# Performance work log

Hardware: AMD Instinct MI355X
Metric: run time of the kernel (lower is better)

## Reference

```python
import jax, jax.numpy as jnp
import numpy as np

H = 32          # query heads
KV = 8          # kv heads
DH = 64         # head dim
WINDOW = 1024   # sliding window
BASE = 10000.0  # rope base


def _rope(x, pos):
    """Interleaved RoPE as in RotaryEmbedding.apply. x: (B,H,T,Dh), pos: (T,)."""
    inv = 1.0 / (BASE ** (jnp.arange(0, DH, 2, dtype=jnp.float32) / DH))  # (Dh/2,)
    freqs = pos.astype(jnp.float32)[:, None] * inv[None, :]               # (T, Dh/2)
    cos = jnp.cos(freqs)[None, None].astype(x.dtype)
    sin = jnp.sin(freqs)[None, None].astype(x.dtype)
    x1, x2 = x[..., ::2], x[..., 1::2]
    o1 = x1 * cos - x2 * sin
    o2 = x1 * sin + x2 * cos
    return jnp.stack([o1, o2], axis=-1).reshape(x.shape)


def setup_inputs() -> dict:
    key = jax.random.key(0)
    ks = jax.random.split(key, 5)
    B, T, D, Tc = 2, 4096, 2048, 4096
    x = jax.random.normal(ks[0], (B, T, D), jnp.float32)
    k_cache = jax.random.normal(ks[1], (B, KV, Tc, DH), jnp.float32)
    v_cache = jax.random.normal(ks[2], (B, KV, Tc, DH), jnp.float32)
    Wq = jax.random.normal(ks[3], (D, D), jnp.float32) * 0.02
    Wo = jax.random.normal(ks[4], (D, D), jnp.float32) * 0.02
    return {"x": x, "k_cache": k_cache, "v_cache": v_cache, "Wq": Wq, "Wo": Wo}


def reference(x, k_cache, v_cache, Wq, Wo):
    """AttnLayer.forward, role='follower', local=True, return_attn=False, eval mode."""
    B, T, D = x.shape
    rep = H // KV
    # q projection: nn.Linear(d, H*Dh, bias=False) -> x @ W.T
    q = (x @ Wq.T).reshape(B, T, H, DH).transpose(0, 2, 1, 3)  # (B,H,T,Dh)
    Tc = k_cache.shape[2]
    pos_q = jnp.arange(Tc - T, Tc)
    q = _rope(q, pos_q)
    # GQA: KV -> H head replication (repeat_interleave along head dim)
    k = jnp.repeat(k_cache, rep, axis=1)  # (B,H,Tc,Dh)
    v = jnp.repeat(v_cache, rep, axis=1)
    # sliding-window slice: keep last `window` keys
    w = min(WINDOW, Tc)
    k = k[:, :, Tc - w:, :]  # (B,H,Tk,Dh)
    v = v[:, :, Tc - w:, :]
    Tk = w
    scale = 1.0 / np.sqrt(DH).astype(np.float32)
    scores = jnp.einsum('bhtd,bhsd->bhts', q, k) * scale  # (B,H,T,Tk)
    # torch SDPA is_causal with L != S uses a TOP-LEFT aligned tril mask: j <= i
    causal = jnp.arange(Tk)[None, :] <= jnp.arange(T)[:, None]  # (T,Tk)
    scores = jnp.where(causal[None, None], scores, -jnp.inf)
    attn = jax.nn.softmax(scores, axis=-1)
    out = jnp.einsum('bhts,bhsd->bhtd', attn, v)
    out = out.transpose(0, 2, 1, 3).reshape(B, T, H * DH)
    return out @ Wo.T
```

## Files before the change

kernel.cpp:

```cpp
#include <hip/hip_runtime.h>
#include <math.h>

typedef __attribute__((ext_vector_type(8))) short short8;
typedef __attribute__((ext_vector_type(4))) float floatx4;
typedef __attribute__((ext_vector_type(4))) unsigned int uintx4;
typedef __attribute__((ext_vector_type(2))) unsigned int uintx2;

#define MFMA16(a, b, c) __builtin_amdgcn_mfma_f32_16x16x32_bf16((a), (b), (c), 0, 0, 0)

#define QSCALE 0.18033688011112042f

__device__ __forceinline__ unsigned short f2bf(float x) {
    unsigned int u = __float_as_uint(x);
    u += 0x7fffu + ((u >> 16) & 1u);
    return (unsigned short)(u >> 16);
}

__device__ __forceinline__ short8 lds8(const unsigned short* p) {
    return *reinterpret_cast<const short8*>(p);
}

__device__ __forceinline__ void g2l16(const unsigned short* g, unsigned short* l) {
    __builtin_amdgcn_global_load_lds(
        (const __attribute__((address_space(1))) unsigned int*)g,
        (__attribute__((address_space(3))) unsigned int*)l,
        16, 0, 0);
}

__device__ __forceinline__ unsigned int cvtpk(float a, float b) {
    unsigned int r;
    asm("v_cvt_pk_bf16_f32 %0, %1, %2" : "=v"(r) : "v"(a), "v"(b));
    return r;
}

__device__ __forceinline__ void pl32swap(unsigned int& a, unsigned int& b) {
    asm("v_permlane32_swap_b32 %0, %1" : "+v"(a), "+v"(b));
}

__device__ __forceinline__ void pl16swap(unsigned int& a, unsigned int& b) {
    asm("v_permlane16_swap_b32 %0, %1" : "+v"(a), "+v"(b));
}

__global__ void cvt_bf16(const float* __restrict__ src, unsigned short* __restrict__ dst, int n4) {
    int i = blockIdx.x * blockDim.x + threadIdx.x;
    if (i >= n4) return;
    float4 v = reinterpret_cast<const float4*>(src)[i];
    ushort4 o;
    o.x = f2bf(v.x); o.y = f2bf(v.y); o.z = f2bf(v.z); o.w = f2bf(v.w);
    reinterpret_cast<ushort4*>(dst)[i] = o;
}

__global__ void prep_k(const float* __restrict__ kc, unsigned short* __restrict__ Kw) {
    int i = blockIdx.x * blockDim.x + threadIdx.x;
    int d4  = (i & 15) * 4;
    int s   = (i >> 4) & 1023;
    int bkv = i >> 14;
    size_t src = ((size_t)bkv * 4096 + 3072 + s) * 64 + d4;
    float4 kv = *reinterpret_cast<const float4*>(kc + src);
    ushort4 ko;
    ko.x = f2bf(kv.x); ko.y = f2bf(kv.y); ko.z = f2bf(kv.z); ko.w = f2bf(kv.w);
    *reinterpret_cast<ushort4*>(Kw + ((size_t)bkv * 1024 + s) * 64 + d4) = ko;
}

__global__ void prep_v(const float* __restrict__ vc, unsigned short* __restrict__ Vt) {
    __shared__ unsigned short tl[64][72];
    const int bkv = blockIdx.x >> 4;
    const int s0  = (blockIdx.x & 15) * 64;
    const int t   = threadIdx.x;
    const int sl  = t >> 2;
    const int dq  = (t & 3) * 16;
    const float* src = vc + ((size_t)bkv * 4096 + 3072 + s0 + sl) * 64 + dq;
    float4 v0 = reinterpret_cast<const float4*>(src)[0];
    float4 v1 = reinterpret_cast<const float4*>(src)[1];
    float4 v2 = reinterpret_cast<const float4*>(src)[2];
    float4 v3 = reinterpret_cast<const float4*>(src)[3];
    tl[dq +  0][sl] = f2bf(v0.x); tl[dq +  1][sl] = f2bf(v0.y);
    tl[dq +  2][sl] = f2bf(v0.z); tl[dq +  3][sl] = f2bf(v0.w);
    tl[dq +  4][sl] = f2bf(v1.x); tl[dq +  5][sl] = f2bf(v1.y);
    tl[dq +  6][sl] = f2bf(v1.z); tl[dq +  7][sl] = f2bf(v1.w);
    tl[dq +  8][sl] = f2bf(v2.x); tl[dq +  9][sl] = f2bf(v2.y);
    tl[dq + 10][sl] = f2bf(v2.z); tl[dq + 11][sl] = f2bf(v2.w);
    tl[dq + 12][sl] = f2bf(v3.x); tl[dq + 13][sl] = f2bf(v3.y);
    tl[dq + 14][sl] = f2bf(v3.z); tl[dq + 15][sl] = f2bf(v3.w);
    __syncthreads();
    const int dl = t >> 2;
    const int sc = (t & 3) * 16;
    unsigned short* dst = Vt + ((size_t)bkv * 64 + dl) * 1024 + s0 + sc;
    short8 x0 = *reinterpret_cast<const short8*>(&tl[dl][sc]);
    short8 x1 = *reinterpret_cast<const short8*>(&tl[dl][sc + 8]);
    *reinterpret_cast<short8*>(dst)     = x0;
    *reinterpret_cast<short8*>(dst + 8) = x1;
}

template <int EPI>
__global__ __launch_bounds__(256)
void gemm_bt(const unsigned short* __restrict__ A,
             const unsigned short* __restrict__ Bt,
             float* __restrict__ Cf,
             unsigned short* __restrict__ Cb) {
    constexpr int K = 2048;
    __shared__ unsigned short As[128 * 32];
    __shared__ unsigned short Bs[128 * 32];
    __shared__ float2 tab[EPI == 0 ? 128 * 33 : 1];

    const int tid  = threadIdx.x;
    const int lane = tid & 63;
    const int l15  = lane & 15;
    const int quad = lane >> 4;
    const int wid  = tid >> 6;
    const int wm   = (wid & 1) * 64;
    const int wn   = (wid >> 1) * 64;

    const int bn = blockIdx.x & 15;
    const int bm = blockIdx.x >> 4;

    if (EPI == 0) {
        const int t0 = (bm & 31) * 128;
        for (int e = tid; e < 4096; e += 256) {
            int tl = e >> 5, d2 = e & 31;
            float f = (float)(t0 + tl) * exp2f(-(float)d2 * 0.41524101186092f);
            float sn, cs; __sincosf(f, &sn, &cs);
            tab[tl * 33 + d2] = make_float2(cs, sn);
        }
    }

    const int row0 = tid >> 2;
    const int kc8  = (tid & 3) * 8;
    const unsigned short* Ag0 = A  + (size_t)(bm * 128 + row0) * K + kc8;
    const unsigned short* Ag1 = Ag0 + (size_t)64 * K;
    const unsigned short* Bg0 = Bt + (size_t)(bn * 128 + row0) * K + kc8;
    const unsigned short* Bg1 = Bg0 + (size_t)64 * K;
    unsigned short* AsW0 = As + wid * 512;
    unsigned short* AsW1 = As + 2048 + wid * 512;
    unsigned short* BsW0 = Bs + wid * 512;
    unsigned short* BsW1 = Bs + 2048 + wid * 512;

    floatx4 c00 = {0,0,0,0}, c01 = {0,0,0,0}, c02 = {0,0,0,0}, c03 = {0,0,0,0};
    floatx4 c10 = {0,0,0,0}, c11 = {0,0,0,0}, c12 = {0,0,0,0}, c13 = {0,0,0,0};
    floatx4 c20 = {0,0,0,0}, c21 = {0,0,0,0}, c22 = {0,0,0,0}, c23 = {0,0,0,0};
    floatx4 c30 = {0,0,0,0}, c31 = {0,0,0,0}, c32 = {0,0,0,0}, c33 = {0,0,0,0};

    for (int k0 = 0; k0 < K; k0 += 32) {
        __syncthreads();
        g2l16(Ag0 + k0, AsW0);
        g2l16(Ag1 + k0, AsW1);
        g2l16(Bg0 + k0, BsW0);
        g2l16(Bg1 + k0, BsW1);
        __syncthreads();

        short8 a0 = lds8(&As[(wm +  0 + l15) * 32 + quad * 8]);
        short8 a1 = lds8(&As[(wm + 16 + l15) * 32 + quad * 8]);
        short8 a2 = lds8(&As[(wm + 32 + l15) * 32 + quad * 8]);
        short8 a3 = lds8(&As[(wm + 48 + l15) * 32 + quad * 8]);
        short8 b0 = lds8(&Bs[(wn +  0 + l15) * 32 + quad * 8]);
        short8 b1 = lds8(&Bs[(wn + 16 + l15) * 32 + quad * 8]);
        short8 b2 = lds8(&Bs[(wn + 32 + l15) * 32 + quad * 8]);
        short8 b3 = lds8(&Bs[(wn + 48 + l15) * 32 + quad * 8]);

        c00 = MFMA16(a0, b0, c00); c01 = MFMA16(a0, b1, c01);
        c02 = MFMA16(a0, b2, c02); c03 = MFMA16(a0, b3, c03);
        c10 = MFMA16(a1, b0, c10); c11 = MFMA16(a1, b1, c11);
        c12 = MFMA16(a1, b2, c12); c13 = MFMA16(a1, b3, c13);
        c20 = MFMA16(a2, b0, c20); c21 = MFMA16(a2, b1, c21);
        c22 = MFMA16(a2, b2, c22); c23 = MFMA16(a2, b3, c23);
        c30 = MFMA16(a3, b0, c30); c31 = MFMA16(a3, b1, c31);
        c32 = MFMA16(a3, b2, c32); c33 = MFMA16(a3, b3, c33);
    }

#define EPI_TILE(i, j, C) do {                                                  \
    _Pragma("unroll")                                                           \
    for (int r = 0; r < 4; ++r) {                                               \
        int row = bm * 128 + wm + (i) * 16 + quad * 4 + r;                      \
        int col = bn * 128 + wn + (j) * 16 + l15;                               \
        float v = (C)[r];                                                       \
        if (EPI == 0) {                                                         \
            float p = __shfl_xor(v, 1);                                         \
            int t = row & 4095, b = row >> 12;                                  \
            int hh = col >> 6, d = col & 63;                                    \
            int tl = wm + (i) * 16 + quad * 4 + r;                              \
            float2 cspair = tab[tl * 33 + (d >> 1)];                            \
            float o = (d & 1) ? (p * cspair.y + v * cspair.x)                   \
                              : (v * cspair.x - p * cspair.y);                  \
            o *= QSCALE;                                                        \
            float po = __shfl_xor(o, 1);                                        \
            if (!(lane & 1)) {                                                  \
                unsigned int pk = (unsigned int)f2bf(o) |                       \
                                  ((unsigned int)f2bf(po) << 16);               \
                *reinterpret_cast<unsigned int*>(                               \
                    Cb + ((size_t)((b * 32 + hh) * 4096 + t)) * 64 + d) = pk;   \
            }                                                                   \
        } else {                                                                \
            Cf[(size_t)row * 2048 + col] = v;                                   \
        }                                                                       \
    }                                                                           \
} while (0)

    EPI_TILE(0, 0, c00); EPI_TILE(0, 1, c01); EPI_TILE(0, 2, c02); EPI_TILE(0, 3, c03);
    EPI_TILE(1, 0, c10); EPI_TILE(1, 1, c11); EPI_TILE(1, 2, c12); EPI_TILE(1, 3, c13);
    EPI_TILE(2, 0, c20); EPI_TILE(2, 1, c21); EPI_TILE(2, 2, c22); EPI_TILE(2, 3, c23);
    EPI_TILE(3, 0, c30); EPI_TILE(3, 1, c31); EPI_TILE(3, 2, c32); EPI_TILE(3, 3, c33);
#undef EPI_TILE
}

__global__ __launch_bounds__(512, 8)
void attn(const unsigned short* __restrict__ Q,
          const unsigned short* __restrict__ Kw,
          const unsigned short* __restrict__ Vt,
          unsigned short* __restrict__ O) {
    const int blk  = blockIdx.x;
    const int qblk = blk & 31;
    const int bh   = blk >> 5;
    const int h    = bh & 31;
    const int b    = bh >> 5;
    const int kvh  = h >> 2;

    const int tid  = threadIdx.x;
    const int lane = tid & 63;
    const int l15  = lane & 15;
    const int quad = lane >> 4;
    const int wid  = tid >> 6;
    const int qt0  = qblk * 128 + wid * 16;

    const unsigned short* Qp = Q  + ((size_t)bh * 4096 + qt0) * 64;
    const unsigned short* Kp = Kw + (size_t)(b * 8 + kvh) * 1024 * 64;
    const unsigned short* Vp = Vt + (size_t)(b * 8 + kvh) * 64 * 1024;

    __shared__ unsigned short Ks[2][4096];
    __shared__ unsigned short Vs[2][4096];

    short8 qa0 = lds8(&Qp[l15 * 64 + quad * 8]);
    short8 qa1 = lds8(&Qp[l15 * 64 + 32 + quad * 8]);

    const unsigned short* gK = Kp + (size_t)((wid >> 1) * 16 + l15) * 64
                                  + (wid & 1) * 32 + quad * 8;
    const unsigned short* gV = Vp + (size_t)((wid >> 1) * 16 + l15) * 1024
                                  + (wid & 1) * 32 + quad * 8;
    unsigned short* sK0 = &Ks[0][wid * 512];
    unsigned short* sK1 = &Ks[1][wid * 512];
    unsigned short* sV0 = &Vs[0][wid * 512];
    unsigned short* sV1 = &Vs[1][wid * 512];

    const int ntiles = (qblk < 7 ? 2 * qblk + 2 : 16);
    const int nkW    = (qt0 + 16 < 1024) ? qt0 + 16 : 1024;
    const int ntW    = (nkW + 63) >> 6;
    const bool diagW = (qt0 < 1024);

    g2l16(gK, sK0);
    g2l16(gV, sV0);

    floatx4 o0 = {0,0,0,0}, o1 = {0,0,0,0}, o2 = {0,0,0,0}, o3 = {0,0,0,0};
    float Lq = 0.f;
    float m = -INFINITY;

    for (int it = 0; it < ntiles; ++it) {
        __syncthreads();
        const int cur = it & 1;
        if (it + 1 < ntiles) {
            g2l16(gK + (it + 1) * 4096, cur ? sK0 : sK1);
            g2l16(gV + (it + 1) * 64,   cur ? sV0 : sV1);
        }
        if (it >= ntW) continue;
        const int s0 = it << 6;
        const unsigned short* Kc = Ks[cur];
        const unsigned short* Vc = Vs[cur];

        floatx4 sS[4];
#pragma unroll
        for (int c = 0; c < 4; ++c) {
            floatx4 z = {0, 0, 0, 0};
            z = MFMA16(lds8(Kc + c * 1024 + lane * 8), qa0, z);
            z = MFMA16(lds8(Kc + c * 1024 + 512 + lane * 8), qa1, z);
            sS[c] = z;
        }

        const bool last = (it == ntW - 1);
        bool skipHi = false;
        if (last && diagW) {
#pragma unroll
            for (int c = 0; c < 4; ++c)
#pragma unroll
                for (int r = 0; r < 4; ++r)
                    if (s0 + c * 16 + quad * 4 + r > qt0 + l15) sS[c][r] = -INFINITY;
            skipHi = (nkW - s0 <= 32);
        }

        float t0 = fmaxf(fmaxf(sS[0][0], sS[0][1]), fmaxf(sS[0][2], sS[0][3]));
        float t1 = fmaxf(fmaxf(sS[1][0], sS[1][1]), fmaxf(sS[1][2], sS[1][3]));
        float t2 = fmaxf(fmaxf(sS[2][0], sS[2][1]), fmaxf(sS[2][2], sS[2][3]));
        float t3 = fmaxf(fmaxf(sS[3][0], sS[3][1]), fmaxf(sS[3][2], sS[3][3]));
        float mx = fmaxf(fmaxf(t0, t1), fmaxf(t2, t3));
        mx = fmaxf(mx, __shfl_xor(mx, 16));
        mx = fmaxf(mx, __shfl_xor(mx, 32));

        if (!__all(mx <= m + 8.0f)) {
            const float mn = fmaxf(m, mx);
            const float alpha = exp2f(m - mn);
            m = mn;
            o0 *= alpha; o1 *= alpha; o2 *= alpha; o3 *= alpha;
            Lq *= alpha;
        }

        float p[4][4];
#pragma unroll
        for (int c = 0; c < 4; ++c)
#pragma unroll
            for (int r = 0; r < 4; ++r) p[c][r] = exp2f(sS[c][r] - m);
        Lq += ((p[0][0] + p[0][1] + p[0][2] + p[0][3]) + (p[1][0] + p[1][1] + p[1][2] + p[1][3]))
            + ((p[2][0] + p[2][1] + p[2][2] + p[2][3]) + (p[3][0] + p[3][1] + p[3][2] + p[3][3]));

        unsigned int a0 = cvtpk(p[0][0], p[0][1]);
        unsigned int a1 = cvtpk(p[0][2], p[0][3]);
        unsigned int a2 = cvtpk(p[1][0], p[1][1]);
        unsigned int a3 = cvtpk(p[1][2], p[1][3]);
        pl32swap(a0, a2); pl32swap(a1, a3);
        pl16swap(a0, a2); pl16swap(a1, a3);
        uintx4 tlo = {a0, a1, a2, a3};
        short8 pa_lo = __builtin_bit_cast(short8, tlo);

        o0 = MFMA16(lds8(Vc + 0 * 512 + lane * 8), pa_lo, o0);
        o1 = MFMA16(lds8(Vc + 2 * 512 + lane * 8), pa_lo, o1);
        o2 = MFMA16(lds8(Vc + 4 * 512 + lane * 8), pa_lo, o2);
        o3 = MFMA16(lds8(Vc + 6 * 512 + lane * 8), pa_lo, o3);
        if (!skipHi) {
            unsigned int b0 = cvtpk(p[2][0], p[2][1]);
            unsigned int b1 = cvtpk(p[2][2], p[2][3]);
            unsigned int b2 = cvtpk(p[3][0], p[3][1]);
            unsigned int b3 = cvtpk(p[3][2], p[3][3]);
            pl32swap(b0, b2); pl32swap(b1, b3);
            pl16swap(b0, b2); pl16swap(b1, b3);
            uintx4 thi = {b0, b1, b2, b3};
            short8 pa_hi = __builtin_bit_cast(short8, thi);
            o0 = MFMA16(lds8(Vc + 1 * 512 + lane * 8), pa_hi, o0);
            o1 = MFMA16(lds8(Vc + 3 * 512 + lane * 8), pa_hi, o1);
            o2 = MFMA16(lds8(Vc + 5 * 512 + lane * 8), pa_hi, o2);
            o3 = MFMA16(lds8(Vc + 7 * 512 + lane * 8), pa_hi, o3);
        }
    }

    Lq += __shfl_xor(Lq, 16);
    Lq += __shfl_xor(Lq, 32);
    const float inv = 1.f / Lq;

    unsigned short* Op = O + (size_t)b * 4096 * 2048 + (size_t)(qt0 + l15) * 2048
                           + h * 64 + quad * 4;
    uintx2 w0, w1, w2, w3;
    w0.x = cvtpk(o0[0] * inv, o0[1] * inv); w0.y = cvtpk(o0[2] * inv, o0[3] * inv);
    w1.x = cvtpk(o1[0] * inv, o1[1] * inv); w1.y = cvtpk(o1[2] * inv, o1[3] * inv);
    w2.x = cvtpk(o2[0] * inv, o2[1] * inv); w2.y = cvtpk(o2[2] * inv, o2[3] * inv);
    w3.x = cvtpk(o3[0] * inv, o3[1] * inv); w3.y = cvtpk(o3[2] * inv, o3[3] * inv);
    *reinterpret_cast<uintx2*>(Op)      = w0;
    *reinterpret_cast<uintx2*>(Op + 16) = w1;
    *reinterpret_cast<uintx2*>(Op + 32) = w2;
    *reinterpret_cast<uintx2*>(Op + 48) = w3;
}

extern "C" void kernel_launch(void* const* d_in, const int* in_sizes, int n_in,
                              void* d_out, int out_size, void* d_ws, size_t ws_size,
                              hipStream_t stream) {
    const float* x  = (const float*)d_in[0];
    const float* kc = (const float*)d_in[1];
    const float* vc = (const float*)d_in[2];
    const float* Wq = (const float*)d_in[3];
    const float* Wo = (const float*)d_in[4];
    float* out = (float*)d_out;

    char* ws = (char*)d_ws;
    unsigned short* Xb  = (unsigned short*)(ws);
    unsigned short* Qb  = (unsigned short*)(ws + 33554432);
    unsigned short* Wqb = (unsigned short*)(ws + 67108864);
    unsigned short* Wob = (unsigned short*)(ws + 75497472);
    unsigned short* Kwb = (unsigned short*)(ws + 83886080);
    unsigned short* Vtb = (unsigned short*)(ws + 85983232);

    cvt_bf16<<<16384, 256, 0, stream>>>(x,  Xb,  4194304);
    cvt_bf16<<<4096,  256, 0, stream>>>(Wq, Wqb, 1048576);
    cvt_bf16<<<4096,  256, 0, stream>>>(Wo, Wob, 1048576);
    prep_k<<<1024, 256, 0, stream>>>(kc, Kwb);
    prep_v<<<256, 256, 0, stream>>>(vc, Vtb);

    gemm_bt<0><<<1024, 256, 0, stream>>>(Xb, Wqb, nullptr, Qb);
    attn<<<2048, 512, 0, stream>>>(Qb, Kwb, Vtb, Xb);
    gemm_bt<1><<<1024, 256, 0, stream>>>(Xb, Wob, out, nullptr);
}
```

Measured before the change: 505.8 us.

## Replace GEMM with 256x256-tile double-buffered kernel using async LDS loads

```diff
diff --git a/kernel.cpp b/kernel.cpp
--- a/kernel.cpp
+++ b/kernel.cpp
@@ -93,113 +93,124 @@
 }
 
 template <int EPI>
-__global__ __launch_bounds__(256)
-void gemm_bt(const unsigned short* __restrict__ A,
+__global__ __launch_bounds__(512, 2)
+void gemm256(const unsigned short* __restrict__ A,
              const unsigned short* __restrict__ Bt,
              float* __restrict__ Cf,
              unsigned short* __restrict__ Cb) {
-    constexpr int K = 2048;
-    __shared__ unsigned short As[128 * 32];
-    __shared__ unsigned short Bs[128 * 32];
-    __shared__ float2 tab[EPI == 0 ? 128 * 33 : 1];
+    constexpr int K  = 2048;
+    constexpr int NT = 64;
+    __shared__ unsigned short sm[32768];
 
     const int tid  = threadIdx.x;
     const int lane = tid & 63;
     const int l15  = lane & 15;
     const int quad = lane >> 4;
     const int wid  = tid >> 6;
-    const int wm   = (wid & 1) * 64;
-    const int wn   = (wid >> 1) * 64;
-
-    const int bn = blockIdx.x & 15;
-    const int bm = blockIdx.x >> 4;
-
+    const int wr   = wid >> 2;
+    const int wc   = wid & 3;
+
+    const int bn = blockIdx.x & 7;
+    const int bm = blockIdx.x >> 3;
+
+    const unsigned short* gA0 = A  + (size_t)(bm * 256 + 2 * wid * 16 + l15) * K + quad * 8;
+    const unsigned short* gA1 = gA0 + (size_t)16 * K;
+    const unsigned short* gB0 = Bt + (size_t)(bn * 256 + 2 * wid * 16 + l15) * K + quad * 8;
+    const unsigned short* gB1 = gB0 + (size_t)16 * K;
+
+    auto STAGE = [&](int t) {
+        unsigned short* dst = sm + (t & 1) * 16384 + 2 * wid * 512;
+        const int off = t * 32;
+        g2l16(gA0 + off, dst);
+        g2l16(gA1 + off, dst + 512);
+        g2l16(gB0 + off, dst + 8192);
+        g2l16(gB1 + off, dst + 8704);
+    };
+
+    floatx4 acc[8][4];
+#pragma unroll
+    for (int i = 0; i < 8; ++i)
+#pragma unroll
+        for (int j = 0; j < 4; ++j) acc[i][j] = floatx4{0, 0, 0, 0};
+
+    STAGE(0);
+    STAGE(1);
+    asm volatile("s_waitcnt vmcnt(4)" ::: "memory");
+    __builtin_amdgcn_s_barrier();
+    asm volatile("" ::: "memory");
+
+    for (int t = 0; t < NT; ++t) {
+        const unsigned short* cb = sm + (t & 1) * 16384;
+
+        short8 bf[4], af[8];
+#pragma unroll
+        for (int j = 0; j < 4; ++j)
+            bf[j] = lds8(cb + 8192 + (wc * 4 + j) * 512 + lane * 8);
+#pragma unroll
+        for (int i = 0; i < 8; ++i)
+            af[i] = lds8(cb + (wr * 8 + i) * 512 + lane * 8);
+
+        asm volatile("s_waitcnt lgkmcnt(0)" ::: "memory");
+        __builtin_amdgcn_s_barrier();
+        asm volatile("" ::: "memory");
+
+        if (t + 2 < NT) STAGE(t + 2);
+
+        __builtin_amdgcn_s_setprio(1);
+#pragma unroll
+        for (int i = 0; i < 8; ++i)
+#pragma unroll
+            for (int j = 0; j < 4; ++j)
+                acc[i][j] = MFMA16(af[i], bf[j], acc[i][j]);
+        __builtin_amdgcn_s_setprio(0);
+
+        if (t + 2 < NT) asm volatile("s_waitcnt vmcnt(4)" ::: "memory");
+        else            asm volatile("s_waitcnt vmcnt(0)" ::: "memory");
+        __builtin_amdgcn_s_barrier();
+        asm volatile("" ::: "memory");
+    }
+
+    float2* tabf = reinterpret_cast<float2*>(sm);
     if (EPI == 0) {
-        const int t0 = (bm & 31) * 128;
-        for (int e = tid; e < 4096; e += 256) {
+        const int t0 = (bm & 15) * 256;
+        for (int e = tid; e < 8192; e += 512) {
             int tl = e >> 5, d2 = e & 31;
             float f = (float)(t0 + tl) * exp2f(-(float)d2 * 0.41524101186092f);
             float sn, cs; __sincosf(f, &sn, &cs);
-            tab[tl * 33 + d2] = make_float2(cs, sn);
-        }
+            tabf[tl * 32 + d2] = make_float2(cs, sn);
+        }
+        __syncthreads();
     }
 
-    const int row0 = tid >> 2;
-    const int kc8  = (tid & 3) * 8;
-    const unsigned short* Ag0 = A  + (size_t)(bm * 128 + row0) * K + kc8;
-    const unsigned short* Ag1 = Ag0 + (size_t)64 * K;
-    const unsigned short* Bg0 = Bt + (size_t)(bn * 128 + row0) * K + kc8;
-    const unsigned short* Bg1 = Bg0 + (size_t)64 * K;
-    unsigned short* AsW0 = As + wid * 512;
-    unsigned short* AsW1 = As + 2048 + wid * 512;
-    unsigned short* BsW0 = Bs + wid * 512;
-    unsigned short* BsW1 = Bs + 2048 + wid * 512;
-
-    floatx4 c00 = {0,0,0,0}, c01 = {0,0,0,0}, c02 = {0,0,0,0}, c03 = {0,0,0,0};
-    floatx4 c10 = {0,0,0,0}, c11 = {0,0,0,0}, c12 = {0,0,0,0}, c13 = {0,0,0,0};
-    floatx4 c20 = {0,0,0,0}, c21 = {0,0,0,0}, c22 = {0,0,0,0}, c23 = {0,0,0,0};
-    floatx4 c30 = {0,0,0,0}, c31 = {0,0,0,0}, c32 = {0,0,0,0}, c33 = {0,0,0,0};
-
-    for (int k0 = 0; k0 < K; k0 += 32) {
-        __syncthreads();
-        g2l16(Ag0 + k0, AsW0);
-        g2l16(Ag1 + k0, AsW1);
-        g2l16(Bg0 + k0, BsW0);
-        g2l16(Bg1 + k0, BsW1);
-        __syncthreads();
-
-        short8 a0 = lds8(&As[(wm +  0 + l15) * 32 + quad * 8]);
-        short8 a1 = lds8(&As[(wm + 16 + l15) * 32 + quad * 8]);
-        short8 a2 = lds8(&As[(wm + 32 + l15) * 32 + quad * 8]);
-        short8 a3 = lds8(&As[(wm + 48 + l15) * 32 + quad * 8]);
-        short8 b0 = lds8(&Bs[(wn +  0 + l15) * 32 + quad * 8]);
-        short8 b1 = lds8(&Bs[(wn + 16 + l15) * 32 + quad * 8]);
-        short8 b2 = lds8(&Bs[(wn + 32 + l15) * 32 + quad * 8]);
-        short8 b3 = lds8(&Bs[(wn + 48 + l15) * 32 + quad * 8]);
-
-        c00 = MFMA16(a0, b0, c00); c01 = MFMA16(a0, b1, c01);
-        c02 = MFMA16(a0, b2, c02); c03 = MFMA16(a0, b3, c03);
-        c10 = MFMA16(a1, b0, c10); c11 = MFMA16(a1, b1, c11);
-        c12 = MFMA16(a1, b2, c12); c13 = MFMA16(a1, b3, c13);
-        c20 = MFMA16(a2, b0, c20); c21 = MFMA16(a2, b1, c21);
-        c22 = MFMA16(a2, b2, c22); c23 = MFMA16(a2, b3, c23);
-        c30 = MFMA16(a3, b0, c30); c31 = MFMA16(a3, b1, c31);
-        c32 = MFMA16(a3, b2, c32); c33 = MFMA16(a3, b3, c33);
-    }
-
-#define EPI_TILE(i, j, C) do {                                                  \
-    _Pragma("unroll")                                                           \
-    for (int r = 0; r < 4; ++r) {                                               \
-        int row = bm * 128 + wm + (i) * 16 + quad * 4 + r;                      \
-        int col = bn * 128 + wn + (j) * 16 + l15;                               \
-        float v = (C)[r];                                                       \
-        if (EPI == 0) {                                                         \
-            float p = __shfl_xor(v, 1);                                         \
-            int t = row & 4095, b = row >> 12;                                  \
-            int hh = col >> 6, d = col & 63;                                    \
-            int tl = wm + (i) * 16 + quad * 4 + r;                              \
-            float2 cspair = tab[tl * 33 + (d >> 1)];                            \
-            float o = (d & 1) ? (p * cspair.y + v * cspair.x)                   \
-                              : (v * cspair.x - p * cspair.y);                  \
-            o *= QSCALE;                                                        \
-            float po = __shfl_xor(o, 1);                                        \
-            if (!(lane & 1)) {                                                  \
-                unsigned int pk = (unsigned int)f2bf(o) |                       \
-                                  ((unsigned int)f2bf(po) << 16);               \
-                *reinterpret_cast<unsigned int*>(                               \
-                    Cb + ((size_t)((b * 32 + hh) * 4096 + t)) * 64 + d) = pk;   \
-            }                                                                   \
-        } else {                                                                \
-            Cf[(size_t)row * 2048 + col] = v;                                   \
-        }                                                                       \
-    }                                                                           \
-} while (0)
-
-    EPI_TILE(0, 0, c00); EPI_TILE(0, 1, c01); EPI_TILE(0, 2, c02); EPI_TILE(0, 3, c03);
-    EPI_TILE(1, 0, c10); EPI_TILE(1, 1, c11); EPI_TILE(1, 2, c12); EPI_TILE(1, 3, c13);
-    EPI_TILE(2, 0, c20); EPI_TILE(2, 1, c21); EPI_TILE(2, 2, c22); EPI_TILE(2, 3, c23);
-    EPI_TILE(3, 0, c30); EPI_TILE(3, 1, c31); EPI_TILE(3, 2, c32); EPI_TILE(3, 3, c33);
-#undef EPI_TILE
+#pragma unroll
+    for (int i = 0; i < 8; ++i)
+#pragma unroll
+        for (int j = 0; j < 4; ++j)
+#pragma unroll
+            for (int r = 0; r < 4; ++r) {
+                int row = bm * 256 + wr * 128 + i * 16 + quad * 4 + r;
+                int col = bn * 256 + wc * 64 + j * 16 + l15;
+                float v = acc[i][j][r];
+                if (EPI == 0) {
+                    float p = __shfl_xor(v, 1);
+                    int t_ = row & 4095, b_ = row >> 12;
+                    int hh = col >> 6, d = col & 63;
+                    int tl = wr * 128 + i * 16 + quad * 4 + r;
+                    float2 cspair = tabf[tl * 32 + (d >> 1)];
+                    float o = (d & 1) ? (p * cspair.y + v * cspair.x)
+                                      : (v * cspair.x - p * cspair.y);
+                    o *= QSCALE;
+                    float po = __shfl_xor(o, 1);
+                    if (!(lane & 1)) {
+                        unsigned int pk = (unsigned int)f2bf(o) |
+                                          ((unsigned int)f2bf(po) << 16);
+                        *reinterpret_cast<unsigned int*>(
+                            Cb + ((size_t)((b_ * 32 + hh) * 4096 + t_)) * 64 + d) = pk;
+                    }
+                } else {
+                    Cf[(size_t)row * 2048 + col] = v;
+                }
+            }
 }
 
 __global__ __launch_bounds__(512, 8)
@@ -378,7 +389,7 @@
     prep_k<<<1024, 256, 0, stream>>>(kc, Kwb);
     prep_v<<<256, 256, 0, stream>>>(vc, Vtb);
 
-    gemm_bt<0><<<1024, 256, 0, stream>>>(Xb, Wqb, nullptr, Qb);
+    gemm256<0><<<256, 512, 0, stream>>>(Xb, Wqb, nullptr, Qb);
     attn<<<2048, 512, 0, stream>>>(Qb, Kwb, Vtb, Xb);
-    gemm_bt<1><<<1024, 256, 0, stream>>>(Xb, Wob, out, nullptr);
-}
+    gemm256<1><<<256, 512, 0, stream>>>(Xb, Wob, out, nullptr);
+}
```

Measured after the change: 444.1 us. 12.2% less time.
